# Performance work log

Hardware: AMD Instinct MI355X
Metric: run time of the kernel (lower is better)

## Reference

```python
import jax, jax.numpy as jnp
import numpy as np

NR, NQ, NH, NV = 256, 64, 64, 4
B = 8192
NDRAW = 12
# zoneout probabilities from __init__ (applied deterministically, eval-mode expectation)
ZO_IJ, ZO_ID, ZO_GJ, ZO_GD = 0.3, 0.2, 0.3, 0.2


def _lin_init(key, fan_in, fan_out):
    kw, kb = jax.random.split(key)
    s = 1.0 / np.sqrt(fan_in)
    W = jax.random.uniform(kw, (fan_in, fan_out), jnp.float32, -s, s)
    b = jax.random.uniform(kb, (fan_out,), jnp.float32, -s, s)
    return W, b


def setup_inputs() -> dict:
    key = jax.random.key(0)
    ks = jax.random.split(key, 16)
    inp = {"ndraw": NDRAW}
    inp["cnd_repr"] = jax.random.normal(ks[0], (B, NR), jnp.float32)
    inp["qry_jrep"] = jax.random.normal(ks[1], (B, NQ), jnp.float32)
    inp["qry_drep"] = jax.random.normal(ks[2], (B, NQ), jnp.float32)
    inp["qry_v"] = jax.random.normal(ks[3], (B, NV), jnp.float32)
    for n in ["hi_j", "ci_j", "oi_j", "hi_d", "ci_d", "oi_d",
              "hg_j", "cg_j", "og_j", "hg_d", "cg_d", "og_d", "ug_j", "ug_d"]:
        inp[n] = jnp.zeros((B, NH), jnp.float32)
    # LSTM cells: W [in+nh, 4*nh]
    inp["W_ij"], inp["b_ij"] = _lin_init(ks[4], NR + NQ + NH + NH, 4 * NH)
    inp["W_id"], inp["b_id"] = _lin_init(ks[5], NR + NQ + NH + NH, 4 * NH)
    inp["W_gj"], inp["b_gj"] = _lin_init(ks[6], NR + NH + NH, 4 * NH)
    inp["W_gd"], inp["b_gd"] = _lin_init(ks[7], NR + NH + NV + NH, 4 * NH)
    # GaussianFactor heads: nh -> (mean, logv)
    inp["W_poj"], inp["b_poj"] = _lin_init(ks[8], NH, 2 * NH)
    inp["W_pod"], inp["b_pod"] = _lin_init(ks[9], NH, 2 * NH)
    inp["W_prj"], inp["b_prj"] = _lin_init(ks[10], NH, 2 * NH)
    inp["W_prd"], inp["b_prd"] = _lin_init(ks[11], NH, 2 * NH)
    # GeneratorDelta: cat(u, h) -> delta
    inp["W_dj"], inp["b_dj"] = _lin_init(ks[12], 2 * NH, NH)
    inp["W_dd"], inp["b_dd"] = _lin_init(ks[13], 2 * NH, NH)
    return inp


def _lstm(x, h, c, W, b, zo):
    g = jnp.concatenate([x, h], axis=1) @ W + b  # [B, 4*NH]
    i, f, gg, o = jnp.split(g, 4, axis=1)
    i, f, o = jax.nn.sigmoid(i), jax.nn.sigmoid(f), jax.nn.sigmoid(o)
    c_new = f * c + i * jnp.tanh(gg)
    h_new = o * jnp.tanh(c_new)
    # deterministic zoneout (expectation form)
    return zo * h + (1.0 - zo) * h_new, zo * c + (1.0 - zo) * c_new, o


def _gauss_stats(h, W, b):
    s = h @ W + b
    mean, logv = jnp.split(s, 2, axis=1)
    return mean, logv


def _delta(u, h, W, b):
    return jax.nn.leaky_relu(jnp.concatenate([u, h], axis=1) @ W + b)


def _forward(ndraw, cnd_repr, qry_jrep, qry_drep, qry_v,
             hi_j, ci_j, oi_j, hi_d, ci_d, oi_d,
             hg_j, cg_j, og_j, hg_d, cg_d, og_d, ug_j, ug_d,
             W_ij, b_ij, W_id, b_id, W_gj, b_gj, W_gd, b_gd,
             W_poj, b_poj, W_pod, b_pod, W_prj, b_prj, W_prd, b_prd,
             W_dj, b_dj, W_dd, b_dd):
    Bn = cnd_repr.shape[0]
    eps_j = jax.random.normal(jax.random.key(1), (ndraw, Bn, NH), jnp.float32)
    eps_d = jax.random.normal(jax.random.key(2), (ndraw, Bn, NH), jnp.float32)

    def step(carry, eps):
        (hi_j, ci_j, oi_j, hi_d, ci_d, oi_d,
         hg_j, cg_j, og_j, hg_d, cg_d, og_d, ug_j, ug_d) = carry
        ej, ed = eps
        # priors from current generator states (sampled z unused in loop)
        pr_m_j, pr_v_j = _gauss_stats(hg_j, W_prj, b_prj)
        pr_m_d, pr_v_d = _gauss_stats(hg_d, W_prd, b_prd)
        # inference states
        inp_ij = jnp.concatenate([cnd_repr, qry_jrep, hg_j], axis=1)
        inp_id = jnp.concatenate([cnd_repr, qry_drep, hg_d], axis=1)
        hi_j, ci_j, oi_j = _lstm(inp_ij, hi_j, ci_j, W_ij, b_ij, ZO_IJ)
        hi_d, ci_d, oi_d = _lstm(inp_id, hi_d, ci_d, W_id, b_id, ZO_ID)
        # posteriors + reparameterized samples
        po_m_j, po_v_j = _gauss_stats(hi_j, W_poj, b_poj)
        po_m_d, po_v_d = _gauss_stats(hi_d, W_pod, b_pod)
        z_j = po_m_j + jnp.exp(0.5 * po_v_j) * ej
        z_d = po_m_d + jnp.exp(0.5 * po_v_d) * ed
        # generator states
        inp_gj = jnp.concatenate([cnd_repr, z_j], axis=1)
        inp_gd = jnp.concatenate([cnd_repr, z_d, qry_v], axis=1)
        hg_j, cg_j, og_j = _lstm(inp_gj, hg_j, cg_j, W_gj, b_gj, ZO_GJ)
        hg_d, cg_d, og_d = _lstm(inp_gd, hg_d, cg_d, W_gd, b_gd, ZO_GD)
        # additive canvas updates
        ug_j = ug_j + _delta(ug_j, hg_j, W_dj, b_dj)
        ug_d = ug_d + _delta(ug_d, hg_d, W_dd, b_dd)
        carry = (hi_j, ci_j, oi_j, hi_d, ci_d, oi_d,
                 hg_j, cg_j, og_j, hg_d, cg_d, og_d, ug_j, ug_d)
        ys = (pr_m_j, pr_v_j, pr_m_d, pr_v_d, po_m_j, po_v_j, po_m_d, po_v_d)
        return carry, ys

    carry0 = (hi_j, ci_j, oi_j, hi_d, ci_d, oi_d,
              hg_j, cg_j, og_j, hg_d, cg_d, og_d, ug_j, ug_d)
    carry, ys = jax.lax.scan(step, carry0, (eps_j, eps_d))
    ug_j_out, ug_d_out = carry[-2], carry[-1]
    # pack: [2 + 8*ndraw, B, NH] (canvases then per-draw prior/posterior stats)
    out = jnp.concatenate([ug_j_out[None], ug_d_out[None]] + list(ys), axis=0)
    return out


def reference(ndraw, cnd_repr, qry_jrep, qry_drep, qry_v,
              hi_j, ci_j, oi_j, hi_d, ci_d, oi_d,
              hg_j, cg_j, og_j, hg_d, cg_d, og_d, ug_j, ug_d,
              W_ij, b_ij, W_id, b_id, W_gj, b_gj, W_gd, b_gd,
              W_poj, b_poj, W_pod, b_pod, W_prj, b_prj, W_prd, b_prd,
              W_dj, b_dj, W_dd, b_dd):
    return _forward(ndraw, cnd_repr, qry_jrep, qry_drep, qry_v,
                    hi_j, ci_j, oi_j, hi_d, ci_d, oi_d,
                    hg_j, cg_j, og_j, hg_d, cg_d, og_d, ug_j, ug_d,
                    W_ij, b_ij, W_id, b_id, W_gj, b_gj, W_gd, b_gd,
                    W_poj, b_poj, W_pod, b_pod, W_prj, b_prj, W_prd, b_prd,
                    W_dj, b_dj, W_dd, b_dd)
```

## Files before the change

### kernel.cpp

```cpp
#include <hip/hip_runtime.h>
#include <hip/hip_bf16.h>


#define RROWS 16

typedef __attribute__((ext_vector_type(8))) short bf16x8;
typedef __attribute__((ext_vector_type(4))) float f32x4;

#define MFMA(A, Bv, C) __builtin_amdgcn_mfma_f32_16x16x32_bf16(A, Bv, C, 0, 0, 0)

#define FR_WI   0
#define FR_WG   32768
#define FR_WPR  65536
#define FR_WPO  73728
#define FR_WD   81920
#define FR_SIDE 90112

__device__ __forceinline__ unsigned short f2bf(float f) {
  unsigned u = __float_as_uint(f);
  return (unsigned short)((u + 0x7FFFu + ((u >> 16) & 1u)) >> 16);
}
__device__ __forceinline__ unsigned pk2(float a, float b) {
  return (unsigned)f2bf(a) | ((unsigned)f2bf(b) << 16);
}
__device__ __forceinline__ float sigf(float x) {
  return 1.0f / (1.0f + __expf(-x));
}
__device__ __forceinline__ float tanh_f(float x) {
  return 1.0f - 2.0f / (__expf(2.0f * x) + 1.0f);
}

__device__ __forceinline__ float eps_threefry(unsigned seed, unsigned idx) {
  unsigned x0 = 0u, x1 = idx;
  const unsigned ks0 = 0u, ks1 = seed, ks2 = seed ^ 0x1BD11BDAu;
  x0 += ks0; x1 += ks1;
#define TF_R(r) { x0 += x1; x1 = (x1 << (r)) | (x1 >> (32 - (r))); x1 ^= x0; }
  TF_R(13) TF_R(15) TF_R(26) TF_R(6)  x0 += ks1; x1 += ks2 + 1u;
  TF_R(17) TF_R(29) TF_R(16) TF_R(24) x0 += ks2; x1 += ks0 + 2u;
  TF_R(13) TF_R(15) TF_R(26) TF_R(6)  x0 += ks0; x1 += ks1 + 3u;
  TF_R(17) TF_R(29) TF_R(16) TF_R(24) x0 += ks1; x1 += ks2 + 4u;
  TF_R(13) TF_R(15) TF_R(26) TF_R(6)  x0 += ks2; x1 += ks0 + 5u;
#undef TF_R
  unsigned bits = x0 ^ x1;
  unsigned fb = (bits >> 9) | 0x3F800000u;
  const float lo = -0.99999994f;
  float f = __uint_as_float(fb) - 1.0f;
  float u = fmaxf(lo, f * 2.0f + lo);
  float w = -log1pf(-u * u);
  float p;
  if (w < 5.0f) {
    w -= 2.5f;
    p = 2.81022636e-08f;
    p = fmaf(p, w, 3.43273939e-07f);
    p = fmaf(p, w, -3.5233877e-06f);
    p = fmaf(p, w, -4.39150654e-06f);
    p = fmaf(p, w, 0.00021858087f);
    p = fmaf(p, w, -0.00125372503f);
    p = fmaf(p, w, -0.00417768164f);
    p = fmaf(p, w, 0.246640727f);
    p = fmaf(p, w, 1.50140941f);
  } else {
    w = sqrtf(w) - 3.0f;
    p = -0.000200214257f;
    p = fmaf(p, w, 0.000100950558f);
    p = fmaf(p, w, 0.00134934322f);
    p = fmaf(p, w, -0.00367342844f);
    p = fmaf(p, w, 0.00573950773f);
    p = fmaf(p, w, -0.0076224613f);
    p = fmaf(p, w, 0.00943887047f);
    p = fmaf(p, w, 1.00167406f);
    p = fmaf(p, w, 2.83297682f);
  }
  return 1.41421356f * (p * u);
}

__global__ __launch_bounds__(256) void GeRN_prepEps(
    const float* __restrict__ Wij, const float* __restrict__ Wid,
    const float* __restrict__ Wgj, const float* __restrict__ Wgd,
    const float* __restrict__ Wprj, const float* __restrict__ Wprd,
    const float* __restrict__ Wpoj, const float* __restrict__ Wpod,
    const float* __restrict__ Wdj, const float* __restrict__ Wdd,
    unsigned short* __restrict__ frB, unsigned short* __restrict__ sBs,
    float* __restrict__ ebuf, unsigned ndBN)
{
  if (blockIdx.x < 236) {
    const int vb = blockIdx.x * 4 + (threadIdx.x >> 6);
    const int l = threadIdx.x & 63;
    if (vb < 352) {
      const int s = vb / 176;
      int tt = vb % 176;
      const float* W; int ldw, rb, NT, kt, nt; size_t doff;
      if (tt < 64)       { W = s ? Wid : Wij; ldw = 256; NT = 16; kt = tt >> 4; nt = tt & 15;
                           rb = 320 + kt * 32; doff = FR_WI; }
      else if (tt < 128) { tt -= 64; W = s ? Wgd : Wgj; ldw = 256; NT = 16; kt = tt >> 4; nt = tt & 15;
                           rb = (kt < 2) ? 256 + kt * 32 : (s ? 324 : 320) + (kt - 2) * 32; doff = FR_WG; }
      else if (tt < 144) { tt -= 128; W = s ? Wprd : Wprj; ldw = 128; NT = 8; kt = tt >> 3; nt = tt & 7;
                           rb = kt * 32; doff = FR_WPR; }
      else if (tt < 160) { tt -= 144; W = s ? Wpod : Wpoj; ldw = 128; NT = 8; kt = tt >> 3; nt = tt & 7;
                           rb = kt * 32; doff = FR_WPO; }
      else               { tt -= 160; W = s ? Wdd : Wdj; ldw = 64; NT = 4; kt = tt >> 2; nt = tt & 3;
                           rb = (kt < 2) ? kt * 32 : 64 + (kt - 2) * 32; doff = FR_WD; }
      unsigned short* dst = frB + (size_t)s * FR_SIDE + doff
                          + ((size_t)(kt * NT + nt) * 64 + l) * 8;
      const int kk = (l >> 4) * 8;
      const int c = nt * 16 + (l & 15);
      #pragma unroll
      for (int j = 0; j < 8; ++j)
        dst[j] = f2bf(W[(size_t)(rb + kk + j) * ldw + c]);
    } else {
      int bb = vb - 352;
      int mat, base;
      if (bb < 160)      { mat = 0; base = 0; }
      else if (bb < 320) { mat = 1; base = 160; }
      else if (bb < 448) { mat = 2; base = 320; }
      else               { mat = 3; base = 448; }
      int tt = bb - base;
      int kk = tt >> 4, nt = tt & 15;
      const float* W = mat == 0 ? Wij : mat == 1 ? Wid : mat == 2 ? Wgj : Wgd;
      const int c = nt * 16 + (l & 15);
      const int kl0 = (l >> 4) * 8;
      unsigned short* dst = sBs + ((size_t)bb * 64 + l) * 8;
      if (mat == 3 && kk == 8) {
        #pragma unroll
        for (int j = 0; j < 8; ++j) {
          int klo = kl0 + j;
          dst[j] = (klo < 4) ? f2bf(W[(size_t)(320 + klo) * 256 + c]) : (unsigned short)0;
        }
      } else {
        int rb = (kk < 8) ? kk * 32 : 256 + (kk - 8) * 32;
        #pragma unroll
        for (int j = 0; j < 8; ++j)
          dst[j] = f2bf(W[(size_t)(rb + kl0 + j) * 256 + c]);
      }
    }
  } else {
    unsigned j0 = ((blockIdx.x - 236) * 256u + threadIdx.x) * 8u;
    const unsigned total = 2u * ndBN;
    if (j0 >= total) return;
    const unsigned s = (j0 >= ndBN) ? 1u : 0u;
    const unsigned i0 = j0 - s * ndBN;
    const unsigned seed = 1u + s;
    float v[8];
    #pragma unroll
    for (int k = 0; k < 8; ++k) v[k] = eps_threefry(seed, i0 + (unsigned)k);
    float4 a = {v[0], v[1], v[2], v[3]};
    float4 b = {v[4], v[5], v[6], v[7]};
    *(float4*)(ebuf + j0) = a;
    *(float4*)(ebuf + j0 + 4) = b;
  }
}

__global__ __launch_bounds__(256) void GeRN_staticM(
    const float* __restrict__ cnd, const float* __restrict__ qj,
    const float* __restrict__ qd, const float* __restrict__ qv,
    const float* __restrict__ bij, const float* __restrict__ bid,
    const float* __restrict__ bgj, const float* __restrict__ bgd,
    const unsigned short* __restrict__ sBs,
    float* __restrict__ pre, int B)
{
  alignas(16) __shared__ unsigned short As[13][2][64][8];
  const int tid = threadIdx.x;
  const int l = tid & 63;
  const int wv = tid >> 6;
  const int b0 = blockIdx.x * 32;

  for (int i = tid; i < 32 * 52; i += 256) {
    int r = i / 52, kc = i % 52;
    int mf = r >> 4, rr = r & 15;
    float v[8];
    if (kc < 32) {
      const float4* p = (const float4*)&cnd[(size_t)(b0 + r) * 256 + kc * 8];
      float4 x0 = p[0], x1 = p[1];
      v[0] = x0.x; v[1] = x0.y; v[2] = x0.z; v[3] = x0.w;
      v[4] = x1.x; v[5] = x1.y; v[6] = x1.z; v[7] = x1.w;
    } else if (kc < 40) {
      const float4* p = (const float4*)&qj[(size_t)(b0 + r) * 64 + (kc - 32) * 8];
      float4 x0 = p[0], x1 = p[1];
      v[0] = x0.x; v[1] = x0.y; v[2] = x0.z; v[3] = x0.w;
      v[4] = x1.x; v[5] = x1.y; v[6] = x1.z; v[7] = x1.w;
    } else if (kc < 48) {
      const float4* p = (const float4*)&qd[(size_t)(b0 + r) * 64 + (kc - 40) * 8];
      float4 x0 = p[0], x1 = p[1];
      v[0] = x0.x; v[1] = x0.y; v[2] = x0.z; v[3] = x0.w;
      v[4] = x1.x; v[5] = x1.y; v[6] = x1.z; v[7] = x1.w;
    } else if (kc == 48) {
      #pragma unroll
      for (int j = 0; j < 8; ++j) v[j] = (j < 4) ? qv[(size_t)(b0 + r) * 4 + j] : 0.0f;
    } else {
      #pragma unroll
      for (int j = 0; j < 8; ++j) v[j] = 0.0f;
    }
    int kt = kc >> 2;
    int lane = rr + (kc & 3) * 16;
    uint4 wq;
    wq.x = pk2(v[0], v[1]); wq.y = pk2(v[2], v[3]);
    wq.z = pk2(v[4], v[5]); wq.w = pk2(v[6], v[7]);
    *(uint4*)&As[kt][mf][lane][0] = wq;
  }
  __syncthreads();

  const int colb = wv * 64 + (l & 15);
  const int rowb = (l >> 4) * 4;

  #pragma unroll
  for (int mat = 0; mat < 4; ++mat) {
    const int ktN  = (mat == 2) ? 8 : (mat == 3) ? 9 : 10;
    const int ktB  = mat == 0 ? 0 : mat == 1 ? 160 : mat == 2 ? 320 : 448;
    const float* bv = mat == 0 ? bij : mat == 1 ? bid : mat == 2 ? bgj : bgd;
    f32x4 acc[2][4];
    #pragma unroll
    for (int ntl = 0; ntl < 4; ++ntl) {
      float bb = bv[colb + ntl * 16];
      f32x4 s = {bb, bb, bb, bb};
      acc[0][ntl] = s; acc[1][ntl] = s;
    }
    #pragma unroll
    for (int kk = 0; kk < ktN; ++kk) {
      int ktA = (kk < 8) ? kk : (mat == 0 ? kk : mat == 1 ? kk + 2 : 12);
      bf16x8 a0 = *(const bf16x8*)&As[ktA][0][l][0];
      bf16x8 a1 = *(const bf16x8*)&As[ktA][1][l][0];
      #pragma unroll
      for (int ntl = 0; ntl < 4; ++ntl) {
        bf16x8 bf = *(const bf16x8*)&sBs[((size_t)(ktB + kk * 16 + wv * 4 + ntl) * 64 + l) * 8];
        acc[0][ntl] = MFMA(a0, bf, acc[0][ntl]);
        acc[1][ntl] = MFMA(a1, bf, acc[1][ntl]);
      }
    }
    float* dp = pre + (size_t)mat * B * 256;
    #pragma unroll
    for (int mf = 0; mf < 2; ++mf)
      #pragma unroll
      for (int ntl = 0; ntl < 4; ++ntl)
        #pragma unroll
        for (int r = 0; r < 4; ++r)
          dp[(size_t)(b0 + mf * 16 + rowb + r) * 256 + colb + ntl * 16] = acc[mf][ntl][r];
  }
}

#define WR_FR(buf, row, c, v) \
  fr[buf][(c) >> 5][((row) & 15) + (((c) >> 3) & 3) * 16][(c) & 7] = f2bf(v)
#define LD_FR(buf, kt) (*(const bf16x8*)&fr[buf][kt][l][0])
#define LD_B(off, kt, nt, NT) \
  (*(const bf16x8*)(FB + (off) + (((kt) * (NT) + (nt)) * 64 + l) * 8))
#define LD_H(ph, kt, nt) \
  (*(const bf16x8*)&shH[(ph) * 8192 + (((kt) * 8 + (nt)) * 64 + l) * 8])

template<int USE_EPS>
__global__ __launch_bounds__(256, 2) void GeRN_recur(
    const unsigned short* __restrict__ frB,
    const float* __restrict__ pre_ij, const float* __restrict__ pre_id,
    const float* __restrict__ pre_gj, const float* __restrict__ pre_gd,
    const float* __restrict__ bprj, const float* __restrict__ bprd,
    const float* __restrict__ bpoj, const float* __restrict__ bpod,
    const float* __restrict__ bdj,  const float* __restrict__ bdd,
    const float* __restrict__ hi_j0, const float* __restrict__ ci_j0,
    const float* __restrict__ hi_d0, const float* __restrict__ ci_d0,
    const float* __restrict__ hg_j0, const float* __restrict__ cg_j0,
    const float* __restrict__ hg_d0, const float* __restrict__ cg_d0,
    const float* __restrict__ ug_j0, const float* __restrict__ ug_d0,
    const float* __restrict__ eps_buf, unsigned ndBN,
    float* __restrict__ out, int B, int nd)
{
  alignas(16) __shared__ unsigned short fr[6][2][64][8];
  alignas(16) __shared__ float preL[2][4][4][64][4];
  alignas(16) __shared__ unsigned short shH[16384];

  const int tid = threadIdx.x;
  const int l   = tid & 63;
  const int wv  = tid >> 6;
  const int s   = blockIdx.x & 1;
  const int rbk = blockIdx.x >> 1;
  const int r0  = (l >> 4) * 4;
  const int col = wv * 16 + (l & 15);
  const int bbase = rbk * 16;
  const size_t BN = (size_t)B * 64;

  const float* hi0 = s ? hi_d0 : hi_j0;  const float* ci0 = s ? ci_d0 : ci_j0;
  const float* hg0 = s ? hg_d0 : hg_j0;  const float* cg0 = s ? cg_d0 : cg_j0;
  const float* ug0 = s ? ug_d0 : ug_j0;
  const float* preIg = s ? pre_id : pre_ij;
  const float* preGg = s ? pre_gd : pre_gj;
  const float* BPR = s ? bprd : bprj;
  const float* BPO = s ? bpod : bpoj;
  const float* BD  = s ? bdd  : bdj;
  const unsigned short* FB = frB + (size_t)s * FR_SIDE;

  bf16x8 wi[4][4], wg[4][4], wd[4];
  #pragma unroll
  for (int kt = 0; kt < 4; ++kt) {
    #pragma unroll
    for (int g = 0; g < 4; ++g) {
      wi[kt][g] = LD_B(FR_WI, kt, g * 4 + wv, 16);
      wg[kt][g] = LD_B(FR_WG, kt, g * 4 + wv, 16);
    }
    wd[kt] = LD_B(FR_WD, kt, wv, 4);
  }
  #pragma unroll
  for (int kt = 0; kt < 4; ++kt) {
    #pragma unroll
    for (int g = 0; g < 4; ++g)
      asm volatile("" : "+v"(wi[kt][g]), "+v"(wg[kt][g]));
    asm volatile("" : "+v"(wd[kt]));
  }

  {
    const float4* src = (const float4*)(FB + FR_WPR);
    float4* dst = (float4*)shH;
    for (int i = tid; i < 2048; i += 256) dst[i] = src[i];
  }

  float hi_[4], ci_[4], hg_[4], cg_[4], u_[4];
  #pragma unroll
  for (int r = 0; r < 4; ++r) {
    size_t gi = (size_t)(bbase + r0 + r) * 64 + col;
    hi_[r] = hi0[gi]; ci_[r] = ci0[gi];
    hg_[r] = hg0[gi]; cg_[r] = cg0[gi];
    u_[r]  = ug0[gi];
  }
  const float bprm = BPR[col], bprv = BPR[64 + col];
  const float bpom = BPO[col], bpov = BPO[64 + col];
  const float bd   = BD[col];

  #pragma unroll
  for (int g = 0; g < 4; ++g)
    #pragma unroll
    for (int r = 0; r < 4; ++r) {
      preL[0][g][wv][l][r] = preIg[(size_t)(bbase + r0 + r) * 256 + g * 64 + col];
      preL[1][g][wv][l][r] = preGg[(size_t)(bbase + r0 + r) * 256 + g * 64 + col];
    }
  #pragma unroll
  for (int r = 0; r < 4; ++r) {
    WR_FR(0, r0 + r, col, hi_[r]);
    WR_FR(2, r0 + r, col, hg_[r]);
    WR_FR(4, r0 + r, col, u_[r]);
  }
  __syncthreads();

  const float zo = s ? 0.2f : 0.3f, zo1 = 1.0f - zo;

  const unsigned gi0 = (unsigned)((bbase + r0) * 64 + col);
  float* o_prm = out + (size_t)(2 + (2 * s) * nd) * BN + gi0;
  float* o_prv = out + (size_t)(2 + (2 * s + 1) * nd) * BN + gi0;
  float* o_pom = out + (size_t)(2 + (4 + 2 * s) * nd) * BN + gi0;
  float* o_pov = out + (size_t)(2 + (5 + 2 * s) * nd) * BN + gi0;
  unsigned e0 = gi0;
  const unsigned BNu = (unsigned)BN;
  const unsigned eseed = 1u + (unsigned)s;
  const float* ep = USE_EPS ? (eps_buf + (size_t)s * ndBN + gi0) : (const float*)0;

  for (int t = 0; t < nd; ++t) {
    const int cb = t & 1;
    float epre[4];
    if (USE_EPS) {
      #pragma unroll
      for (int r = 0; r < 4; ++r) epre[r] = ep[r * 64];
    }
    bf16x8 a_hg0 = LD_FR(2, 0), a_hg1 = LD_FR(2, 1);
    bf16x8 a_hi0 = LD_FR(cb, 0), a_hi1 = LD_FR(cb, 1);

    {
      f32x4 am = {bprm, bprm, bprm, bprm};
      f32x4 av = {bprv, bprv, bprv, bprv};
      am = MFMA(a_hg0, LD_H(0, 0, wv), am);
      am = MFMA(a_hg1, LD_H(0, 1, wv), am);
      av = MFMA(a_hg0, LD_H(0, 0, wv + 4), av);
      av = MFMA(a_hg1, LD_H(0, 1, wv + 4), av);
      #pragma unroll
      for (int r = 0; r < 4; ++r) {
        o_prm[r * 64] = am[r];
        o_prv[r * 64] = av[r];
      }
    }
    {
      f32x4 acc[4];
      #pragma unroll
      for (int g = 0; g < 4; ++g) acc[g] = *(const f32x4*)&preL[0][g][wv][l][0];
      #pragma unroll
      for (int g = 0; g < 4; ++g) {
        acc[g] = MFMA(a_hg0, wi[0][g], acc[g]);
        acc[g] = MFMA(a_hg1, wi[1][g], acc[g]);
        acc[g] = MFMA(a_hi0, wi[2][g], acc[g]);
        acc[g] = MFMA(a_hi1, wi[3][g], acc[g]);
      }
      #pragma unroll
      for (int r = 0; r < 4; ++r) {
        float ig = sigf(acc[0][r]), fg = sigf(acc[1][r]);
        float gg = tanh_f(acc[2][r]), og = sigf(acc[3][r]);
        float cn = fmaf(fg, ci_[r], ig * gg);
        float hn = og * tanh_f(cn);
        hi_[r] = fmaf(zo, hi_[r], zo1 * hn);
        ci_[r] = fmaf(zo, ci_[r], zo1 * cn);
        WR_FR(cb ^ 1, r0 + r, col, hi_[r]);
      }
    }
    __syncthreads();

    {
      bf16x8 a0 = LD_FR(cb ^ 1, 0), a1 = LD_FR(cb ^ 1, 1);
      f32x4 am = {bpom, bpom, bpom, bpom};
      f32x4 av = {bpov, bpov, bpov, bpov};
      am = MFMA(a0, LD_H(1, 0, wv), am);
      am = MFMA(a1, LD_H(1, 1, wv), am);
      av = MFMA(a0, LD_H(1, 0, wv + 4), av);
      av = MFMA(a1, LD_H(1, 1, wv + 4), av);
      #pragma unroll
      for (int r = 0; r < 4; ++r) {
        o_pom[r * 64] = am[r];
        o_pov[r * 64] = av[r];
        float e = USE_EPS ? epre[r] : eps_threefry(eseed, e0 + r * 64);
        float z = fmaf(__expf(0.5f * av[r]), e, am[r]);
        WR_FR(3, r0 + r, col, z);
      }
    }
    __syncthreads();

    {
      bf16x8 az0 = LD_FR(3, 0), az1 = LD_FR(3, 1);
      f32x4 acc[4];
      #pragma unroll
      for (int g = 0; g < 4; ++g) acc[g] = *(const f32x4*)&preL[1][g][wv][l][0];
      #pragma unroll
      for (int g = 0; g < 4; ++g) {
        acc[g] = MFMA(az0,   wg[0][g], acc[g]);
        acc[g] = MFMA(az1,   wg[1][g], acc[g]);
        acc[g] = MFMA(a_hg0, wg[2][g], acc[g]);
        acc[g] = MFMA(a_hg1, wg[3][g], acc[g]);
      }
      #pragma unroll
      for (int r = 0; r < 4; ++r) {
        float ig = sigf(acc[0][r]), fg = sigf(acc[1][r]);
        float gg = tanh_f(acc[2][r]), og = sigf(acc[3][r]);
        float cn = fmaf(fg, cg_[r], ig * gg);
        float hn = og * tanh_f(cn);
        hg_[r] = fmaf(zo, hg_[r], zo1 * hn);
        cg_[r] = fmaf(zo, cg_[r], zo1 * cn);
        WR_FR(2, r0 + r, col, hg_[r]);
      }
    }
    __syncthreads();

    {
      bf16x8 au0 = LD_FR(4 + cb, 0), au1 = LD_FR(4 + cb, 1);
      bf16x8 ah0 = LD_FR(2, 0), ah1 = LD_FR(2, 1);
      f32x4 acc = {bd, bd, bd, bd};
      acc = MFMA(au0, wd[0], acc);
      acc = MFMA(au1, wd[1], acc);
      acc = MFMA(ah0, wd[2], acc);
      acc = MFMA(ah1, wd[3], acc);
      #pragma unroll
      for (int r = 0; r < 4; ++r) {
        float a = acc[r];
        float d = a > 0.0f ? a : 0.01f * a;
        u_[r] += d;
        WR_FR(4 + (cb ^ 1), r0 + r, col, u_[r]);
      }
    }
    __syncthreads();

    o_prm += BN; o_prv += BN; o_pom += BN; o_pov += BN;
    e0 += BNu;
    if (USE_EPS) ep += BN;
  }

  #pragma unroll
  for (int r = 0; r < 4; ++r) {
    size_t gi = (size_t)(bbase + r0 + r) * 64 + col;
    out[(size_t)s * BN + gi] = u_[r];
  }
}

extern "C" void kernel_launch(void* const* d_in, const int* in_sizes, int n_in,
                              void* d_out, int out_size, void* d_ws, size_t ws_size,
                              hipStream_t stream)
{
  const float* cnd = (const float*)d_in[1];
  const float* qj  = (const float*)d_in[2];
  const float* qd  = (const float*)d_in[3];
  const float* qv  = (const float*)d_in[4];
  const float* hi_j0 = (const float*)d_in[5];
  const float* ci_j0 = (const float*)d_in[6];
  const float* hi_d0 = (const float*)d_in[8];
  const float* ci_d0 = (const float*)d_in[9];
  const float* hg_j0 = (const float*)d_in[11];
  const float* cg_j0 = (const float*)d_in[12];
  const float* hg_d0 = (const float*)d_in[14];
  const float* cg_d0 = (const float*)d_in[15];
  const float* ug_j0 = (const float*)d_in[17];
  const float* ug_d0 = (const float*)d_in[18];
  const float* Wij = (const float*)d_in[19]; const float* bij = (const float*)d_in[20];
  const float* Wid = (const float*)d_in[21]; const float* bid = (const float*)d_in[22];
  const float* Wgj = (const float*)d_in[23]; const float* bgj = (const float*)d_in[24];
  const float* Wgd = (const float*)d_in[25]; const float* bgd = (const float*)d_in[26];
  const float* Wpoj = (const float*)d_in[27]; const float* bpoj = (const float*)d_in[28];
  const float* Wpod = (const float*)d_in[29]; const float* bpod = (const float*)d_in[30];
  const float* Wprj = (const float*)d_in[31]; const float* bprj = (const float*)d_in[32];
  const float* Wprd = (const float*)d_in[33]; const float* bprd = (const float*)d_in[34];
  const float* Wdj = (const float*)d_in[35]; const float* bdj = (const float*)d_in[36];
  const float* Wdd = (const float*)d_in[37]; const float* bdd = (const float*)d_in[38];

  const int B = in_sizes[1] / 256;
  const int slots = out_size / (B * 64);
  const int nd = (slots - 2) / 8;

  float* ws = (float*)d_ws;
  const size_t preBytes = (size_t)4 * B * 256 * 4;
  unsigned short* frB = (unsigned short*)((char*)d_ws + preBytes);
  unsigned short* sBs = frB + 2 * FR_SIDE;
  size_t epsOff = preBytes + (size_t)2 * FR_SIDE * 2 + (size_t)592 * 512 * 2;
  epsOff = (epsOff + 255) & ~(size_t)255;
  const unsigned ndBN = (unsigned)((size_t)nd * B * 64);
  float* epsBuf = (float*)((char*)d_ws + epsOff);
  const bool useEps = ws_size >= epsOff + (size_t)2 * ndBN * 4;
  float* out = (float*)d_out;

  const int epsBlocks = useEps ? (int)((2u * ndBN + 2047u) / 2048u) : 0;
  GeRN_prepEps<<<236 + epsBlocks, 256, 0, stream>>>(
      Wij, Wid, Wgj, Wgd, Wprj, Wprd, Wpoj, Wpod, Wdj, Wdd, frB, sBs,
      epsBuf, ndBN);
  GeRN_staticM<<<B / 32, 256, 0, stream>>>(
      cnd, qj, qd, qv, bij, bid, bgj, bgd, sBs, ws, B);
  if (useEps) {
    GeRN_recur<1><<<2 * (B / 16), 256, 0, stream>>>(
        frB,
        ws, ws + (size_t)B * 256, ws + (size_t)2 * B * 256, ws + (size_t)3 * B * 256,
        bprj, bprd, bpoj, bpod, bdj, bdd,
        hi_j0, ci_j0, hi_d0, ci_d0, hg_j0, cg_j0, hg_d0, cg_d0, ug_j0, ug_d0,
        epsBuf, ndBN, out, B, nd);
  } else {
    GeRN_recur<0><<<2 * (B / 16), 256, 0, stream>>>(
        frB,
        ws, ws + (size_t)B * 256, ws + (size_t)2 * B * 256, ws + (size_t)3 * B * 256,
        bprj, bprd, bpoj, bpod, bdj, bdd,
        hi_j0, ci_j0, hi_d0, ci_d0, hg_j0, cg_j0, hg_d0, cg_d0, ug_j0, ug_d0,
        (const float*)0, ndBN, out, B, nd);
  }
}
```

Measured before the change: 226.6 us.

## Fuse static input projections into recurrent kernel, keep pre-activations in registers

Removes the separate static-projection kernel that wrote four B×256 fp32 pre-activation buffers to global memory. Each recurrent block now stages its own 16 rows of cnd/query inputs into LDS as bf16 and computes the input-dependent gate pre-activations with MFMA, holding them in registers across all draws. This cuts one launch plus the global write and read-back of the pre buffers. In exchange it adds register pressure in a kernel that has launch bounds of 2 blocks, and it computes the static products in 16-row rather than 32-row tiles.

```diff
diff --git a/kernel.cpp b/kernel.cpp
--- a/kernel.cpp
+++ b/kernel.cpp
@@ -1,8 +1,6 @@
 #include <hip/hip_runtime.h>
 #include <hip/hip_bf16.h>
 
-
-#define RROWS 16
 
 typedef __attribute__((ext_vector_type(8))) short bf16x8;
 typedef __attribute__((ext_vector_type(4))) float f32x4;
@@ -150,106 +148,23 @@
   }
 }
 
-__global__ __launch_bounds__(256) void GeRN_staticM(
-    const float* __restrict__ cnd, const float* __restrict__ qj,
-    const float* __restrict__ qd, const float* __restrict__ qv,
-    const float* __restrict__ bij, const float* __restrict__ bid,
-    const float* __restrict__ bgj, const float* __restrict__ bgd,
-    const unsigned short* __restrict__ sBs,
-    float* __restrict__ pre, int B)
-{
-  alignas(16) __shared__ unsigned short As[13][2][64][8];
-  const int tid = threadIdx.x;
-  const int l = tid & 63;
-  const int wv = tid >> 6;
-  const int b0 = blockIdx.x * 32;
-
-  for (int i = tid; i < 32 * 52; i += 256) {
-    int r = i / 52, kc = i % 52;
-    int mf = r >> 4, rr = r & 15;
-    float v[8];
-    if (kc < 32) {
-      const float4* p = (const float4*)&cnd[(size_t)(b0 + r) * 256 + kc * 8];
-      float4 x0 = p[0], x1 = p[1];
-      v[0] = x0.x; v[1] = x0.y; v[2] = x0.z; v[3] = x0.w;
-      v[4] = x1.x; v[5] = x1.y; v[6] = x1.z; v[7] = x1.w;
-    } else if (kc < 40) {
-      const float4* p = (const float4*)&qj[(size_t)(b0 + r) * 64 + (kc - 32) * 8];
-      float4 x0 = p[0], x1 = p[1];
-      v[0] = x0.x; v[1] = x0.y; v[2] = x0.z; v[3] = x0.w;
-      v[4] = x1.x; v[5] = x1.y; v[6] = x1.z; v[7] = x1.w;
-    } else if (kc < 48) {
-      const float4* p = (const float4*)&qd[(size_t)(b0 + r) * 64 + (kc - 40) * 8];
-      float4 x0 = p[0], x1 = p[1];
-      v[0] = x0.x; v[1] = x0.y; v[2] = x0.z; v[3] = x0.w;
-      v[4] = x1.x; v[5] = x1.y; v[6] = x1.z; v[7] = x1.w;
-    } else if (kc == 48) {
-      #pragma unroll
-      for (int j = 0; j < 8; ++j) v[j] = (j < 4) ? qv[(size_t)(b0 + r) * 4 + j] : 0.0f;
-    } else {
-      #pragma unroll
-      for (int j = 0; j < 8; ++j) v[j] = 0.0f;
-    }
-    int kt = kc >> 2;
-    int lane = rr + (kc & 3) * 16;
-    uint4 wq;
-    wq.x = pk2(v[0], v[1]); wq.y = pk2(v[2], v[3]);
-    wq.z = pk2(v[4], v[5]); wq.w = pk2(v[6], v[7]);
-    *(uint4*)&As[kt][mf][lane][0] = wq;
-  }
-  __syncthreads();
-
-  const int colb = wv * 64 + (l & 15);
-  const int rowb = (l >> 4) * 4;
-
-  #pragma unroll
-  for (int mat = 0; mat < 4; ++mat) {
-    const int ktN  = (mat == 2) ? 8 : (mat == 3) ? 9 : 10;
-    const int ktB  = mat == 0 ? 0 : mat == 1 ? 160 : mat == 2 ? 320 : 448;
-    const float* bv = mat == 0 ? bij : mat == 1 ? bid : mat == 2 ? bgj : bgd;
-    f32x4 acc[2][4];
-    #pragma unroll
-    for (int ntl = 0; ntl < 4; ++ntl) {
-      float bb = bv[colb + ntl * 16];
-      f32x4 s = {bb, bb, bb, bb};
-      acc[0][ntl] = s; acc[1][ntl] = s;
-    }
-    #pragma unroll
-    for (int kk = 0; kk < ktN; ++kk) {
-      int ktA = (kk < 8) ? kk : (mat == 0 ? kk : mat == 1 ? kk + 2 : 12);
-      bf16x8 a0 = *(const bf16x8*)&As[ktA][0][l][0];
-      bf16x8 a1 = *(const bf16x8*)&As[ktA][1][l][0];
-      #pragma unroll
-      for (int ntl = 0; ntl < 4; ++ntl) {
-        bf16x8 bf = *(const bf16x8*)&sBs[((size_t)(ktB + kk * 16 + wv * 4 + ntl) * 64 + l) * 8];
-        acc[0][ntl] = MFMA(a0, bf, acc[0][ntl]);
-        acc[1][ntl] = MFMA(a1, bf, acc[1][ntl]);
-      }
-    }
-    float* dp = pre + (size_t)mat * B * 256;
-    #pragma unroll
-    for (int mf = 0; mf < 2; ++mf)
-      #pragma unroll
-      for (int ntl = 0; ntl < 4; ++ntl)
-        #pragma unroll
-        for (int r = 0; r < 4; ++r)
-          dp[(size_t)(b0 + mf * 16 + rowb + r) * 256 + colb + ntl * 16] = acc[mf][ntl][r];
-  }
-}
-
 #define WR_FR(buf, row, c, v) \
   fr[buf][(c) >> 5][((row) & 15) + (((c) >> 3) & 3) * 16][(c) & 7] = f2bf(v)
 #define LD_FR(buf, kt) (*(const bf16x8*)&fr[buf][kt][l][0])
 #define LD_B(off, kt, nt, NT) \
   (*(const bf16x8*)(FB + (off) + (((kt) * (NT) + (nt)) * 64 + l) * 8))
+#define LD_S(idx) (*(const bf16x8*)&sBs[((size_t)(idx) * 64 + l) * 8])
 #define LD_H(ph, kt, nt) \
   (*(const bf16x8*)&shH[(ph) * 8192 + (((kt) * 8 + (nt)) * 64 + l) * 8])
 
 template<int USE_EPS>
 __global__ __launch_bounds__(256, 2) void GeRN_recur(
     const unsigned short* __restrict__ frB,
-    const float* __restrict__ pre_ij, const float* __restrict__ pre_id,
-    const float* __restrict__ pre_gj, const float* __restrict__ pre_gd,
+    const unsigned short* __restrict__ sBs,
+    const float* __restrict__ cnd, const float* __restrict__ qjg,
+    const float* __restrict__ qdg, const float* __restrict__ qvg,
+    const float* __restrict__ bij, const float* __restrict__ bid,
+    const float* __restrict__ bgj, const float* __restrict__ bgd,
     const float* __restrict__ bprj, const float* __restrict__ bprd,
     const float* __restrict__ bpoj, const float* __restrict__ bpod,
     const float* __restrict__ bdj,  const float* __restrict__ bdd,
@@ -262,8 +177,8 @@
     float* __restrict__ out, int B, int nd)
 {
   alignas(16) __shared__ unsigned short fr[6][2][64][8];
-  alignas(16) __shared__ float preL[2][4][4][64][4];
   alignas(16) __shared__ unsigned short shH[16384];
+  alignas(16) __shared__ unsigned short As[11][64][8];
 
   const int tid = threadIdx.x;
   const int l   = tid & 63;
@@ -278,11 +193,12 @@
   const float* hi0 = s ? hi_d0 : hi_j0;  const float* ci0 = s ? ci_d0 : ci_j0;
   const float* hg0 = s ? hg_d0 : hg_j0;  const float* cg0 = s ? cg_d0 : cg_j0;
   const float* ug0 = s ? ug_d0 : ug_j0;
-  const float* preIg = s ? pre_id : pre_ij;
-  const float* preGg = s ? pre_gd : pre_gj;
   const float* BPR = s ? bprd : bprj;
   const float* BPO = s ? bpod : bpoj;
   const float* BD  = s ? bdd  : bdj;
+  const float* BI  = s ? bid  : bij;
+  const float* BG  = s ? bgd  : bgj;
+  const float* qq  = s ? qdg  : qjg;
   const unsigned short* FB = frB + (size_t)s * FR_SIDE;
 
   bf16x8 wi[4][4], wg[4][4], wd[4];
@@ -308,6 +224,63 @@
     float4* dst = (float4*)shH;
     for (int i = tid; i < 2048; i += 256) dst[i] = src[i];
   }
+  for (int i = tid; i < 16 * 44; i += 256) {
+    int r = i / 44, kc = i % 44;
+    float v[8];
+    if (kc < 32) {
+      const float4* p = (const float4*)&cnd[(size_t)(bbase + r) * 256 + kc * 8];
+      float4 x0 = p[0], x1 = p[1];
+      v[0] = x0.x; v[1] = x0.y; v[2] = x0.z; v[3] = x0.w;
+      v[4] = x1.x; v[5] = x1.y; v[6] = x1.z; v[7] = x1.w;
+    } else if (kc < 40) {
+      const float4* p = (const float4*)&qq[(size_t)(bbase + r) * 64 + (kc - 32) * 8];
+      float4 x0 = p[0], x1 = p[1];
+      v[0] = x0.x; v[1] = x0.y; v[2] = x0.z; v[3] = x0.w;
+      v[4] = x1.x; v[5] = x1.y; v[6] = x1.z; v[7] = x1.w;
+    } else if (kc == 40 && s) {
+      #pragma unroll
+      for (int j = 0; j < 8; ++j) v[j] = (j < 4) ? qvg[(size_t)(bbase + r) * 4 + j] : 0.0f;
+    } else {
+      #pragma unroll
+      for (int j = 0; j < 8; ++j) v[j] = 0.0f;
+    }
+    int kt = kc >> 2;
+    int lane = r + (kc & 3) * 16;
+    uint4 wq;
+    wq.x = pk2(v[0], v[1]); wq.y = pk2(v[2], v[3]);
+    wq.z = pk2(v[4], v[5]); wq.w = pk2(v[6], v[7]);
+    *(uint4*)&As[kt][lane][0] = wq;
+  }
+  __syncthreads();
+
+  f32x4 preI[4], preG[4];
+  {
+    const int ktB_I = s ? 160 : 0;
+    const int ktB_G = s ? 448 : 320;
+    const int ktN_G = s ? 9 : 8;
+    #pragma unroll
+    for (int g = 0; g < 4; ++g) {
+      float bi = BI[g * 64 + col];
+      float bg = BG[g * 64 + col];
+      f32x4 vi = {bi, bi, bi, bi};
+      f32x4 vg = {bg, bg, bg, bg};
+      preI[g] = vi; preG[g] = vg;
+    }
+    #pragma unroll
+    for (int kk = 0; kk < 10; ++kk) {
+      bf16x8 a = *(const bf16x8*)&As[kk][l][0];
+      #pragma unroll
+      for (int g = 0; g < 4; ++g)
+        preI[g] = MFMA(a, LD_S(ktB_I + kk * 16 + g * 4 + wv), preI[g]);
+    }
+    for (int kk = 0; kk < ktN_G; ++kk) {
+      int ktA = (kk < 8) ? kk : 10;
+      bf16x8 a = *(const bf16x8*)&As[ktA][l][0];
+      #pragma unroll
+      for (int g = 0; g < 4; ++g)
+        preG[g] = MFMA(a, LD_S(ktB_G + kk * 16 + g * 4 + wv), preG[g]);
+    }
+  }
 
   float hi_[4], ci_[4], hg_[4], cg_[4], u_[4];
   #pragma unroll
@@ -321,13 +294,6 @@
   const float bpom = BPO[col], bpov = BPO[64 + col];
   const float bd   = BD[col];
 
-  #pragma unroll
-  for (int g = 0; g < 4; ++g)
-    #pragma unroll
-    for (int r = 0; r < 4; ++r) {
-      preL[0][g][wv][l][r] = preIg[(size_t)(bbase + r0 + r) * 256 + g * 64 + col];
-      preL[1][g][wv][l][r] = preGg[(size_t)(bbase + r0 + r) * 256 + g * 64 + col];
-    }
   #pragma unroll
   for (int r = 0; r < 4; ++r) {
     WR_FR(0, r0 + r, col, hi_[r]);
@@ -374,7 +340,7 @@
     {
       f32x4 acc[4];
       #pragma unroll
-      for (int g = 0; g < 4; ++g) acc[g] = *(const f32x4*)&preL[0][g][wv][l][0];
+      for (int g = 0; g < 4; ++g) acc[g] = preI[g];
       #pragma unroll
       for (int g = 0; g < 4; ++g) {
         acc[g] = MFMA(a_hg0, wi[0][g], acc[g]);
@@ -418,7 +384,7 @@
       bf16x8 az0 = LD_FR(3, 0), az1 = LD_FR(3, 1);
       f32x4 acc[4];
       #pragma unroll
-      for (int g = 0; g < 4; ++g) acc[g] = *(const f32x4*)&preL[1][g][wv][l][0];
+      for (int g = 0; g < 4; ++g) acc[g] = preG[g];
       #pragma unroll
       for (int g = 0; g < 4; ++g) {
         acc[g] = MFMA(az0,   wg[0][g], acc[g]);
@@ -502,11 +468,9 @@
   const int slots = out_size / (B * 64);
   const int nd = (slots - 2) / 8;
 
-  float* ws = (float*)d_ws;
-  const size_t preBytes = (size_t)4 * B * 256 * 4;
-  unsigned short* frB = (unsigned short*)((char*)d_ws + preBytes);
+  unsigned short* frB = (unsigned short*)d_ws;
   unsigned short* sBs = frB + 2 * FR_SIDE;
-  size_t epsOff = preBytes + (size_t)2 * FR_SIDE * 2 + (size_t)592 * 512 * 2;
+  size_t epsOff = (size_t)2 * FR_SIDE * 2 + (size_t)592 * 512 * 2;
   epsOff = (epsOff + 255) & ~(size_t)255;
   const unsigned ndBN = (unsigned)((size_t)nd * B * 64);
   float* epsBuf = (float*)((char*)d_ws + epsOff);
@@ -517,19 +481,15 @@
   GeRN_prepEps<<<236 + epsBlocks, 256, 0, stream>>>(
       Wij, Wid, Wgj, Wgd, Wprj, Wprd, Wpoj, Wpod, Wdj, Wdd, frB, sBs,
       epsBuf, ndBN);
-  GeRN_staticM<<<B / 32, 256, 0, stream>>>(
-      cnd, qj, qd, qv, bij, bid, bgj, bgd, sBs, ws, B);
   if (useEps) {
     GeRN_recur<1><<<2 * (B / 16), 256, 0, stream>>>(
-        frB,
-        ws, ws + (size_t)B * 256, ws + (size_t)2 * B * 256, ws + (size_t)3 * B * 256,
+        frB, sBs, cnd, qj, qd, qv, bij, bid, bgj, bgd,
         bprj, bprd, bpoj, bpod, bdj, bdd,
         hi_j0, ci_j0, hi_d0, ci_d0, hg_j0, cg_j0, hg_d0, cg_d0, ug_j0, ug_d0,
         epsBuf, ndBN, out, B, nd);
   } else {
     GeRN_recur<0><<<2 * (B / 16), 256, 0, stream>>>(
-        frB,
-        ws, ws + (size_t)B * 256, ws + (size_t)2 * B * 256, ws + (size_t)3 * B * 256,
+        frB, sBs, cnd, qj, qd, qv, bij, bid, bgj, bgd,
         bprj, bprd, bpoj, bpod, bdj, bdd,
         hi_j0, ci_j0, hi_d0, ci_d0, hg_j0, cg_j0, hg_d0, cg_d0, ug_j0, ug_d0,
         (const float*)0, ndBN, out, B, nd);
```

Result: faster. 204.6 us (-9.7%).
